# Kernel tuning notes

Measured on AMD Instinct MI355X. Metric: run time of the kernel, lower is better.

## Reference

```python
import jax, jax.numpy as jnp
import numpy as np

B, T, C, D = 8, 4096, 1024, 64  # batch, block_size, input_dim, output_dim


def setup_inputs() -> dict:
    key = jax.random.key(0)
    kx, kk, kq, kv = jax.random.split(key, 4)
    s = 1.0 / np.sqrt(C)  # nn.Linear default init range scale
    X = jax.random.normal(kx, (B, T, C), dtype=jnp.float32)
    Wk = jax.random.uniform(kk, (D, C), jnp.float32, -s, s) * 0.01  # key weight scaled by 0.01 per __post_init__
    Wq = jax.random.uniform(kq, (D, C), jnp.float32, -s, s)
    Wv = jax.random.uniform(kv, (D, C), jnp.float32, -s, s)
    return {"X": X, "Wk": Wk, "Wq": Wq, "Wv": Wv}


def reference(X, Wk, Wq, Wv):
    # bias-free linear projections (torch Linear: X @ W.T)
    keys = jnp.einsum('btc,dc->btd', X, Wk)
    queries = jnp.einsum('btc,dc->btd', X, Wq)
    values = jnp.einsum('btc,dc->btd', X, Wv)
    # scaled dot-product logits [B, T, T]
    logits = jnp.einsum('btd,bsd->bts', queries, keys) / jnp.sqrt(jnp.float32(D))
    causal = jnp.tril(jnp.ones((T, T), dtype=bool))
    logits = jnp.where(causal[None, :, :], logits, -jnp.inf)
    affinities = jax.nn.softmax(logits, axis=2)  # dropout_frac=0.0 -> identity
    return jnp.einsum('bts,bsd->btd', affinities, values)
```

## Files before the change

kernel.cpp:

```cpp
#include <hip/hip_runtime.h>


typedef short bf16x8 __attribute__((ext_vector_type(8)));
typedef short bf16x4 __attribute__((ext_vector_type(4)));
typedef float f32x4  __attribute__((ext_vector_type(4)));

static __device__ __forceinline__ short f2bf(float x) {
    union { float f; unsigned u; } v; v.f = x;
    return (short)((v.u + 0x7fffu + ((v.u >> 16) & 1u)) >> 16);
}

__global__ __launch_bounds__(256, 2) void proj_kernel(
    const float* __restrict__ X,
    const float* __restrict__ Wk, const float* __restrict__ Wq,
    const float* __restrict__ Wv,
    short* __restrict__ Kb,
    short* __restrict__ Qb,
    short* __restrict__ Vt)
{
    __shared__ __align__(16) short xs[2][64 * 72];
    const int tid  = threadIdx.x;
    const int w    = tid >> 6;
    const int lane = tid & 63;
    const int l15  = lane & 15;
    const int quad = lane >> 4;
    const int t0   = blockIdx.x * 64;

    const int rowA = tid >> 3, colg = tid & 7;
    const int rowB = rowA + 32;
    const float* xpA = X + (long)(t0 + rowA) * 1024 + colg * 8;
    const float* xpB = X + (long)(t0 + rowB) * 1024 + colg * 8;
    const int lwA = rowA * 72 + colg * 8;
    const int lwB = rowB * 72 + colg * 8;

    const float* wbase[3];
    wbase[0] = Wk + (long)(w * 16 + l15) * 1024 + quad * 8;
    wbase[1] = Wq + (long)(w * 16 + l15) * 1024 + quad * 8;
    wbase[2] = Wv + (long)(w * 16 + l15) * 1024 + quad * 8;

    f32x4 acc[4][3];
#pragma unroll
    for (int rt = 0; rt < 4; ++rt)
#pragma unroll
        for (int m = 0; m < 3; ++m) { acc[rt][m][0]=0.f; acc[rt][m][1]=0.f; acc[rt][m][2]=0.f; acc[rt][m][3]=0.f; }

    f32x4 xr[2][4];
    bf16x8 wfc[3][2], wfn[3][2];

    {
#pragma unroll
        for (int s = 0; s < 2; ++s) {
            const int k0 = s * 64;
            xr[s][0] = *(const f32x4*)(xpA + k0);
            xr[s][1] = *(const f32x4*)(xpA + k0 + 4);
            xr[s][2] = *(const f32x4*)(xpB + k0);
            xr[s][3] = *(const f32x4*)(xpB + k0 + 4);
        }
#pragma unroll
        for (int m = 0; m < 3; ++m) {
            const float sc = (m == 1) ? 0.18033688f : 1.0f;
#pragma unroll
            for (int k2 = 0; k2 < 2; ++k2) {
                f32x4 w0 = *(const f32x4*)(wbase[m] + k2 * 32);
                f32x4 w1 = *(const f32x4*)(wbase[m] + k2 * 32 + 4);
                bf16x8 f;
#pragma unroll
                for (int j = 0; j < 4; ++j) { f[j] = f2bf(w0[j] * sc); f[j + 4] = f2bf(w1[j] * sc); }
                wfc[m][k2] = f;
            }
        }
        bf16x8 c0, c1;
#pragma unroll
        for (int j = 0; j < 4; ++j) { c0[j] = f2bf(xr[0][0][j]); c0[j+4] = f2bf(xr[0][1][j]);
                                      c1[j] = f2bf(xr[0][2][j]); c1[j+4] = f2bf(xr[0][3][j]); }
        *(bf16x8*)(&xs[0][lwA]) = c0;
        *(bf16x8*)(&xs[0][lwB]) = c1;
    }
    __syncthreads();

#pragma unroll 2
    for (int ks = 0; ks < 16; ++ks) {
        const int buf = ks & 1;
        if (ks < 14) {
            const int k0 = (ks + 2) * 64;
            xr[buf][0] = *(const f32x4*)(xpA + k0);
            xr[buf][1] = *(const f32x4*)(xpA + k0 + 4);
            xr[buf][2] = *(const f32x4*)(xpB + k0);
            xr[buf][3] = *(const f32x4*)(xpB + k0 + 4);
        }
        f32x4 wr[3][2][2];
        if (ks < 15) {
            const int k0 = (ks + 1) * 64;
#pragma unroll
            for (int m = 0; m < 3; ++m)
#pragma unroll
                for (int k2 = 0; k2 < 2; ++k2) {
                    wr[m][k2][0] = *(const f32x4*)(wbase[m] + k0 + k2 * 32);
                    wr[m][k2][1] = *(const f32x4*)(wbase[m] + k0 + k2 * 32 + 4);
                }
        }
#pragma unroll
        for (int k2 = 0; k2 < 2; ++k2)
#pragma unroll
            for (int rt = 0; rt < 4; ++rt) {
                bf16x8 a = *(const bf16x8*)(&xs[buf][(rt * 16 + l15) * 72 + k2 * 32 + quad * 8]);
#pragma unroll
                for (int m = 0; m < 3; ++m)
                    acc[rt][m] = __builtin_amdgcn_mfma_f32_16x16x32_bf16(a, wfc[m][k2], acc[rt][m], 0, 0, 0);
            }
        if (ks < 15) {
#pragma unroll
            for (int m = 0; m < 3; ++m) {
                const float sc = (m == 1) ? 0.18033688f : 1.0f;
#pragma unroll
                for (int k2 = 0; k2 < 2; ++k2) {
                    bf16x8 f;
#pragma unroll
                    for (int j = 0; j < 4; ++j) { f[j] = f2bf(wr[m][k2][0][j] * sc); f[j + 4] = f2bf(wr[m][k2][1][j] * sc); }
                    wfn[m][k2] = f;
                }
            }
            const int nset = (ks + 1) & 1;
            bf16x8 c0, c1;
#pragma unroll
            for (int j = 0; j < 4; ++j) { c0[j] = f2bf(xr[nset][0][j]); c0[j+4] = f2bf(xr[nset][1][j]);
                                          c1[j] = f2bf(xr[nset][2][j]); c1[j+4] = f2bf(xr[nset][3][j]); }
            *(bf16x8*)(&xs[nset][lwA]) = c0;
            *(bf16x8*)(&xs[nset][lwB]) = c1;
        }
        __syncthreads();
#pragma unroll
        for (int m = 0; m < 3; ++m)
#pragma unroll
            for (int k2 = 0; k2 < 2; ++k2) wfc[m][k2] = wfn[m][k2];
    }

    const int d    = w * 16 + l15;
    const int bidx = t0 >> 12;
#pragma unroll
    for (int rt = 0; rt < 4; ++rt) {
        const int tf = t0 + rt * 16 + quad * 4;
#pragma unroll
        for (int r = 0; r < 4; ++r) Kb[(long)(tf + r) * 64 + d] = f2bf(acc[rt][0][r]);
#pragma unroll
        for (int r = 0; r < 4; ++r) Qb[(long)(tf + r) * 64 + d] = f2bf(acc[rt][1][r]);
        bf16x4 pv;
#pragma unroll
        for (int r = 0; r < 4; ++r) pv[r] = f2bf(acc[rt][2][r]);
        *(bf16x4*)(Vt + ((long)bidx * 64 + d) * 4096 + (tf & 4095)) = pv;
    }
}

__global__ __launch_bounds__(256, 2) void flash_kernel(
    const short* __restrict__ Qb,
    const short* __restrict__ Kb,
    const short* __restrict__ Vt,
    float* __restrict__ Out)
{
    __shared__ __align__(16) char smem[33280];
    short* ps = (short*)smem;
    float* os = (float*)smem;
    float* ls = (float*)(smem + 32768);

    const int tid  = threadIdx.x;
    const int w    = tid >> 6;
    const int lane = tid & 63;
    const int l15  = lane & 15;
    const int quad = lane >> 4;
    const int b    = blockIdx.x & 7;
    const int tile = 127 - (blockIdx.x >> 3);
    const int t0   = tile * 32;

    const int nkb = (t0 >> 6) + 1;
    const int len = (nkb + 3) >> 2;
    const int kb0 = w * len;
    const int kb1 = (kb0 + len < nkb) ? (kb0 + len) : nkb;

    const short* Kbase = Kb + (long)b * 4096 * 64;
    const short* Vbase = Vt + (long)b * 64 * 4096;

    bf16x8 aq[2][2];
#pragma unroll
    for (int q2 = 0; q2 < 2; ++q2) {
        const long qoff = ((long)b * 4096 + t0 + q2 * 16 + l15) * 64;
        aq[q2][0] = *(const bf16x8*)(Qb + qoff + quad * 8);
        aq[q2][1] = *(const bf16x8*)(Qb + qoff + 32 + quad * 8);
    }

    bf16x8 bones;
#pragma unroll
    for (int j = 0; j < 8; ++j) bones[j] = (l15 == 0) ? (short)0x3F80 : (short)0;

    f32x4 o[2][4], lacc[2];
#pragma unroll
    for (int q2 = 0; q2 < 2; ++q2) {
        lacc[q2][0]=0.f; lacc[q2][1]=0.f; lacc[q2][2]=0.f; lacc[q2][3]=0.f;
#pragma unroll
        for (int dt = 0; dt < 4; ++dt) { o[q2][dt][0]=0.f; o[q2][dt][1]=0.f; o[q2][dt][2]=0.f; o[q2][dt][3]=0.f; }
    }

    bf16x8 kc[4][2], kn[4][2];
    if (kb0 < kb1) {
        const int s0 = kb0 << 6;
#pragma unroll
        for (int ct = 0; ct < 4; ++ct) {
            const short* kp = Kbase + (long)(s0 + ct * 16 + l15) * 64 + quad * 8;
            kc[ct][0] = *(const bf16x8*)(kp);
            kc[ct][1] = *(const bf16x8*)(kp + 32);
        }
    }

    for (int kb = kb0; kb < kb1; ++kb) {
        const int s0 = kb << 6;

        bf16x8 vf[4][2];
#pragma unroll
        for (int dt = 0; dt < 4; ++dt) {
            const short* vp = Vbase + (long)(dt * 16 + l15) * 4096 + s0 + quad * 8;
            vf[dt][0] = *(const bf16x8*)(vp);
            vf[dt][1] = *(const bf16x8*)(vp + 32);
        }
        if (kb + 1 < kb1) {
            const int sn = s0 + 64;
#pragma unroll
            for (int ct = 0; ct < 4; ++ct) {
                const short* kp = Kbase + (long)(sn + ct * 16 + l15) * 64 + quad * 8;
                kn[ct][0] = *(const bf16x8*)(kp);
                kn[ct][1] = *(const bf16x8*)(kp + 32);
            }
        }

#pragma unroll
        for (int q2 = 0; q2 < 2; ++q2) {
            short* myps = ps + ((w << 1) | q2) * 1152;
            f32x4 st[4];
#pragma unroll
            for (int ct = 0; ct < 4; ++ct) {
                f32x4 z; z[0]=0.f; z[1]=0.f; z[2]=0.f; z[3]=0.f;
                z = __builtin_amdgcn_mfma_f32_16x16x32_bf16(aq[q2][0], kc[ct][0], z, 0, 0, 0);
                st[ct] = __builtin_amdgcn_mfma_f32_16x16x32_bf16(aq[q2][1], kc[ct][1], st[ct] = z, 0, 0, 0);
            }
            if (kb == nkb - 1) {
#pragma unroll
                for (int ct = 0; ct < 4; ++ct) {
                    const int s = s0 + ct * 16 + l15;
#pragma unroll
                    for (int r = 0; r < 4; ++r)
                        if (s > t0 + q2 * 16 + quad * 4 + r) st[ct][r] = -1e30f;
                }
            }
#pragma unroll
            for (int ct = 0; ct < 4; ++ct)
#pragma unroll
                for (int r = 0; r < 4; ++r)
                    myps[(quad * 4 + r) * 72 + ct * 16 + l15] =
                        f2bf(__builtin_amdgcn_exp2f(st[ct][r]));
            bf16x8 ap0 = *(const bf16x8*)(myps + l15 * 72 + quad * 8);
            bf16x8 ap1 = *(const bf16x8*)(myps + l15 * 72 + 32 + quad * 8);
            lacc[q2] = __builtin_amdgcn_mfma_f32_16x16x32_bf16(ap0, bones, lacc[q2], 0, 0, 0);
            lacc[q2] = __builtin_amdgcn_mfma_f32_16x16x32_bf16(ap1, bones, lacc[q2], 0, 0, 0);
#pragma unroll
            for (int dt = 0; dt < 4; ++dt) {
                o[q2][dt] = __builtin_amdgcn_mfma_f32_16x16x32_bf16(ap0, vf[dt][0], o[q2][dt], 0, 0, 0);
                o[q2][dt] = __builtin_amdgcn_mfma_f32_16x16x32_bf16(ap1, vf[dt][1], o[q2][dt], 0, 0, 0);
            }
        }
#pragma unroll
        for (int ct = 0; ct < 4; ++ct) { kc[ct][0] = kn[ct][0]; kc[ct][1] = kn[ct][1]; }
    }

    __syncthreads();
#pragma unroll
    for (int q2 = 0; q2 < 2; ++q2) {
#pragma unroll
        for (int dt = 0; dt < 4; ++dt)
#pragma unroll
            for (int r = 0; r < 4; ++r)
                os[w * 2048 + (q2 * 16 + quad * 4 + r) * 64 + dt * 16 + l15] = o[q2][dt][r];
        if (l15 == 0) {
#pragma unroll
            for (int r = 0; r < 4; ++r) ls[w * 32 + q2 * 16 + quad * 4 + r] = lacc[q2][r];
        }
    }
    __syncthreads();

    const int row = tid >> 3, c0 = (tid & 7) * 8;
    f32x4 a0, a1; a0[0]=0.f;a0[1]=0.f;a0[2]=0.f;a0[3]=0.f; a1=a0;
    float lsum = 0.f;
#pragma unroll
    for (int w2 = 0; w2 < 4; ++w2) {
        f32x4 v0 = *(const f32x4*)(os + w2 * 2048 + row * 64 + c0);
        f32x4 v1 = *(const f32x4*)(os + w2 * 2048 + row * 64 + c0 + 4);
        a0[0]+=v0[0]; a0[1]+=v0[1]; a0[2]+=v0[2]; a0[3]+=v0[3];
        a1[0]+=v1[0]; a1[1]+=v1[1]; a1[2]+=v1[2]; a1[3]+=v1[3];
        lsum += ls[w2 * 32 + row];
    }
    const float inv = 1.0f / lsum;
    f32x4 r0, r1;
    r0[0]=a0[0]*inv; r0[1]=a0[1]*inv; r0[2]=a0[2]*inv; r0[3]=a0[3]*inv;
    r1[0]=a1[0]*inv; r1[1]=a1[1]*inv; r1[2]=a1[2]*inv; r1[3]=a1[3]*inv;
    float* op = Out + ((long)b * 4096 + t0 + row) * 64 + c0;
    *(f32x4*)(op)     = r0;
    *(f32x4*)(op + 4) = r1;
}

extern "C" void kernel_launch(void* const* d_in, const int* in_sizes, int n_in,
                              void* d_out, int out_size, void* d_ws, size_t ws_size,
                              hipStream_t stream) {
    const float* X  = (const float*)d_in[0];
    const float* Wk = (const float*)d_in[1];
    const float* Wq = (const float*)d_in[2];
    const float* Wv = (const float*)d_in[3];

    short* ws = (short*)d_ws;
    const long NE = (long)8 * 4096 * 64;
    short* Qb = ws;
    short* Kb = ws + NE;
    short* Vt = ws + 2 * NE;

    proj_kernel<<<512, 256, 0, stream>>>(X, Wk, Wq, Wv, Kb, Qb, Vt);
    flash_kernel<<<1024, 256, 0, stream>>>(Qb, Kb, Vt, (float*)d_out);
}
```

Measured before the change: 291.5 us.

## Pre-convert weights to bf16 and restructure projection to per-wave register tiles

A new small kernel converts Wk/Wq/Wv to bf16 once, folding the query scale in, and the projection kernel reads these bf16 weights directly. The projection kernel no longer stages X through shared memory; each wave now owns 32 rows and computes all 192 output columns, with a 4-deep register prefetch of X. This removes repeated weight conversion and the block-wide barriers, at the cost of more accumulator registers, more redundant global weight traffic and an extra launch. The flash kernel's loop is also reordered to batch both query subtiles' score MFMAs and softmax writes, and launch-bound occupancy hints are dropped.

```diff
diff --git a/kernel.cpp b/kernel.cpp
--- a/kernel.cpp
+++ b/kernel.cpp
@@ -10,148 +10,104 @@
     return (short)((v.u + 0x7fffu + ((v.u >> 16) & 1u)) >> 16);
 }
 
-__global__ __launch_bounds__(256, 2) void proj_kernel(
+__global__ __launch_bounds__(256) void wconv_kernel(
+    const float* __restrict__ Wk, const float* __restrict__ Wq,
+    const float* __restrict__ Wv, short* __restrict__ Wc)
+{
+    const int i = (blockIdx.x * 256 + threadIdx.x) * 4;
+    const int m = i >> 16;
+    const int off = i & 65535;
+    const float* src = (m == 0) ? Wk : (m == 1) ? Wq : Wv;
+    const float s = (m == 1) ? 0.18033688f : 1.0f;
+    f32x4 v = *(const f32x4*)(src + off);
+    bf16x4 o;
+#pragma unroll
+    for (int r = 0; r < 4; ++r) o[r] = f2bf(v[r] * s);
+    *(bf16x4*)(Wc + i) = o;
+}
+
+__global__ __launch_bounds__(256) void proj_kernel(
     const float* __restrict__ X,
-    const float* __restrict__ Wk, const float* __restrict__ Wq,
-    const float* __restrict__ Wv,
+    const short* __restrict__ Wc,
     short* __restrict__ Kb,
     short* __restrict__ Qb,
     short* __restrict__ Vt)
 {
-    __shared__ __align__(16) short xs[2][64 * 72];
     const int tid  = threadIdx.x;
     const int w    = tid >> 6;
     const int lane = tid & 63;
     const int l15  = lane & 15;
     const int quad = lane >> 4;
-    const int t0   = blockIdx.x * 64;
-
-    const int rowA = tid >> 3, colg = tid & 7;
-    const int rowB = rowA + 32;
-    const float* xpA = X + (long)(t0 + rowA) * 1024 + colg * 8;
-    const float* xpB = X + (long)(t0 + rowB) * 1024 + colg * 8;
-    const int lwA = rowA * 72 + colg * 8;
-    const int lwB = rowB * 72 + colg * 8;
-
-    const float* wbase[3];
-    wbase[0] = Wk + (long)(w * 16 + l15) * 1024 + quad * 8;
-    wbase[1] = Wq + (long)(w * 16 + l15) * 1024 + quad * 8;
-    wbase[2] = Wv + (long)(w * 16 + l15) * 1024 + quad * 8;
-
-    f32x4 acc[4][3];
-#pragma unroll
-    for (int rt = 0; rt < 4; ++rt)
-#pragma unroll
-        for (int m = 0; m < 3; ++m) { acc[rt][m][0]=0.f; acc[rt][m][1]=0.f; acc[rt][m][2]=0.f; acc[rt][m][3]=0.f; }
-
-    f32x4 xr[2][4];
-    bf16x8 wfc[3][2], wfn[3][2];
-
-    {
-#pragma unroll
-        for (int s = 0; s < 2; ++s) {
-            const int k0 = s * 64;
-            xr[s][0] = *(const f32x4*)(xpA + k0);
-            xr[s][1] = *(const f32x4*)(xpA + k0 + 4);
-            xr[s][2] = *(const f32x4*)(xpB + k0);
-            xr[s][3] = *(const f32x4*)(xpB + k0 + 4);
-        }
-#pragma unroll
-        for (int m = 0; m < 3; ++m) {
-            const float sc = (m == 1) ? 0.18033688f : 1.0f;
-#pragma unroll
-            for (int k2 = 0; k2 < 2; ++k2) {
-                f32x4 w0 = *(const f32x4*)(wbase[m] + k2 * 32);
-                f32x4 w1 = *(const f32x4*)(wbase[m] + k2 * 32 + 4);
-                bf16x8 f;
-#pragma unroll
-                for (int j = 0; j < 4; ++j) { f[j] = f2bf(w0[j] * sc); f[j + 4] = f2bf(w1[j] * sc); }
-                wfc[m][k2] = f;
-            }
-        }
-        bf16x8 c0, c1;
-#pragma unroll
-        for (int j = 0; j < 4; ++j) { c0[j] = f2bf(xr[0][0][j]); c0[j+4] = f2bf(xr[0][1][j]);
-                                      c1[j] = f2bf(xr[0][2][j]); c1[j+4] = f2bf(xr[0][3][j]); }
-        *(bf16x8*)(&xs[0][lwA]) = c0;
-        *(bf16x8*)(&xs[0][lwB]) = c1;
-    }
-    __syncthreads();
-
-#pragma unroll 2
-    for (int ks = 0; ks < 16; ++ks) {
-        const int buf = ks & 1;
-        if (ks < 14) {
-            const int k0 = (ks + 2) * 64;
-            xr[buf][0] = *(const f32x4*)(xpA + k0);
-            xr[buf][1] = *(const f32x4*)(xpA + k0 + 4);
-            xr[buf][2] = *(const f32x4*)(xpB + k0);
-            xr[buf][3] = *(const f32x4*)(xpB + k0 + 4);
-        }
-        f32x4 wr[3][2][2];
-        if (ks < 15) {
-            const int k0 = (ks + 1) * 64;
-#pragma unroll
-            for (int m = 0; m < 3; ++m)
-#pragma unroll
-                for (int k2 = 0; k2 < 2; ++k2) {
-                    wr[m][k2][0] = *(const f32x4*)(wbase[m] + k0 + k2 * 32);
-                    wr[m][k2][1] = *(const f32x4*)(wbase[m] + k0 + k2 * 32 + 4);
-                }
-        }
-#pragma unroll
-        for (int k2 = 0; k2 < 2; ++k2)
-#pragma unroll
-            for (int rt = 0; rt < 4; ++rt) {
-                bf16x8 a = *(const bf16x8*)(&xs[buf][(rt * 16 + l15) * 72 + k2 * 32 + quad * 8]);
-#pragma unroll
-                for (int m = 0; m < 3; ++m)
-                    acc[rt][m] = __builtin_amdgcn_mfma_f32_16x16x32_bf16(a, wfc[m][k2], acc[rt][m], 0, 0, 0);
-            }
-        if (ks < 15) {
-#pragma unroll
-            for (int m = 0; m < 3; ++m) {
-                const float sc = (m == 1) ? 0.18033688f : 1.0f;
-#pragma unroll
-                for (int k2 = 0; k2 < 2; ++k2) {
-                    bf16x8 f;
-#pragma unroll
-                    for (int j = 0; j < 4; ++j) { f[j] = f2bf(wr[m][k2][0][j] * sc); f[j + 4] = f2bf(wr[m][k2][1][j] * sc); }
-                    wfn[m][k2] = f;
-                }
-            }
-            const int nset = (ks + 1) & 1;
-            bf16x8 c0, c1;
-#pragma unroll
-            for (int j = 0; j < 4; ++j) { c0[j] = f2bf(xr[nset][0][j]); c0[j+4] = f2bf(xr[nset][1][j]);
-                                          c1[j] = f2bf(xr[nset][2][j]); c1[j+4] = f2bf(xr[nset][3][j]); }
-            *(bf16x8*)(&xs[nset][lwA]) = c0;
-            *(bf16x8*)(&xs[nset][lwB]) = c1;
-        }
-        __syncthreads();
+    const int t0   = blockIdx.x * 128 + w * 32;
+
+    const float* xA = X + (long)(t0 + l15) * 1024 + quad * 8;
+    const float* xB = xA + 16 * 1024;
+    const short* wb = Wc + (long)l15 * 1024 + quad * 8;
+
+    f32x4 acc[2][12];
+#pragma unroll
+    for (int rt = 0; rt < 2; ++rt)
+#pragma unroll
+        for (int t = 0; t < 12; ++t) { acc[rt][t][0]=0.f; acc[rt][t][1]=0.f; acc[rt][t][2]=0.f; acc[rt][t][3]=0.f; }
+
+    f32x4 ar[4][4];
+#pragma unroll
+    for (int d = 0; d < 3; ++d) {
+        ar[d][0] = *(const f32x4*)(xA + d * 32);
+        ar[d][1] = *(const f32x4*)(xA + d * 32 + 4);
+        ar[d][2] = *(const f32x4*)(xB + d * 32);
+        ar[d][3] = *(const f32x4*)(xB + d * 32 + 4);
+    }
+
+#pragma unroll 4
+    for (int ks = 0; ks < 32; ++ks) {
+        const int cur = ks & 3;
+        if (ks + 3 < 32) {
+            const int nxt = (ks + 3) & 3;
+            ar[nxt][0] = *(const f32x4*)(xA + (ks + 3) * 32);
+            ar[nxt][1] = *(const f32x4*)(xA + (ks + 3) * 32 + 4);
+            ar[nxt][2] = *(const f32x4*)(xB + (ks + 3) * 32);
+            ar[nxt][3] = *(const f32x4*)(xB + (ks + 3) * 32 + 4);
+        }
+        bf16x8 bw[12];
 #pragma unroll
         for (int m = 0; m < 3; ++m)
 #pragma unroll
-            for (int k2 = 0; k2 < 2; ++k2) wfc[m][k2] = wfn[m][k2];
-    }
-
-    const int d    = w * 16 + l15;
+            for (int dt = 0; dt < 4; ++dt)
+                bw[m * 4 + dt] = *(const bf16x8*)(wb + m * 65536 + dt * 16384 + ks * 32);
+        bf16x8 a0, a1;
+#pragma unroll
+        for (int j = 0; j < 4; ++j) {
+            a0[j] = f2bf(ar[cur][0][j]); a0[j + 4] = f2bf(ar[cur][1][j]);
+            a1[j] = f2bf(ar[cur][2][j]); a1[j + 4] = f2bf(ar[cur][3][j]);
+        }
+#pragma unroll
+        for (int t = 0; t < 12; ++t) {
+            acc[0][t] = __builtin_amdgcn_mfma_f32_16x16x32_bf16(a0, bw[t], acc[0][t], 0, 0, 0);
+            acc[1][t] = __builtin_amdgcn_mfma_f32_16x16x32_bf16(a1, bw[t], acc[1][t], 0, 0, 0);
+        }
+    }
+
     const int bidx = t0 >> 12;
 #pragma unroll
-    for (int rt = 0; rt < 4; ++rt) {
+    for (int rt = 0; rt < 2; ++rt) {
         const int tf = t0 + rt * 16 + quad * 4;
 #pragma unroll
-        for (int r = 0; r < 4; ++r) Kb[(long)(tf + r) * 64 + d] = f2bf(acc[rt][0][r]);
-#pragma unroll
-        for (int r = 0; r < 4; ++r) Qb[(long)(tf + r) * 64 + d] = f2bf(acc[rt][1][r]);
-        bf16x4 pv;
-#pragma unroll
-        for (int r = 0; r < 4; ++r) pv[r] = f2bf(acc[rt][2][r]);
-        *(bf16x4*)(Vt + ((long)bidx * 64 + d) * 4096 + (tf & 4095)) = pv;
-    }
-}
-
-__global__ __launch_bounds__(256, 2) void flash_kernel(
+        for (int dt = 0; dt < 4; ++dt) {
+            const int d = dt * 16 + l15;
+#pragma unroll
+            for (int r = 0; r < 4; ++r) Kb[(long)(tf + r) * 64 + d] = f2bf(acc[rt][0 + dt][r]);
+#pragma unroll
+            for (int r = 0; r < 4; ++r) Qb[(long)(tf + r) * 64 + d] = f2bf(acc[rt][4 + dt][r]);
+            bf16x4 pv;
+#pragma unroll
+            for (int r = 0; r < 4; ++r) pv[r] = f2bf(acc[rt][8 + dt][r]);
+            *(bf16x4*)(Vt + ((long)bidx * 64 + d) * 4096 + (tf & 4095)) = pv;
+        }
+    }
+}
+
+__global__ __launch_bounds__(256) void flash_kernel(
     const short* __restrict__ Qb,
     const short* __restrict__ Kb,
     const short* __restrict__ Vt,
@@ -230,39 +186,55 @@
             }
         }
 
-#pragma unroll
-        for (int q2 = 0; q2 < 2; ++q2) {
-            short* myps = ps + ((w << 1) | q2) * 1152;
-            f32x4 st[4];
+        f32x4 st[2][4];
+#pragma unroll
+        for (int q2 = 0; q2 < 2; ++q2)
 #pragma unroll
             for (int ct = 0; ct < 4; ++ct) {
                 f32x4 z; z[0]=0.f; z[1]=0.f; z[2]=0.f; z[3]=0.f;
                 z = __builtin_amdgcn_mfma_f32_16x16x32_bf16(aq[q2][0], kc[ct][0], z, 0, 0, 0);
-                st[ct] = __builtin_amdgcn_mfma_f32_16x16x32_bf16(aq[q2][1], kc[ct][1], st[ct] = z, 0, 0, 0);
+                st[q2][ct] = __builtin_amdgcn_mfma_f32_16x16x32_bf16(aq[q2][1], kc[ct][1], z, 0, 0, 0);
             }
-            if (kb == nkb - 1) {
+
+        if (kb == nkb - 1) {
+#pragma unroll
+            for (int q2 = 0; q2 < 2; ++q2)
 #pragma unroll
                 for (int ct = 0; ct < 4; ++ct) {
                     const int s = s0 + ct * 16 + l15;
 #pragma unroll
                     for (int r = 0; r < 4; ++r)
-                        if (s > t0 + q2 * 16 + quad * 4 + r) st[ct][r] = -1e30f;
+                        if (s > t0 + q2 * 16 + quad * 4 + r) st[q2][ct][r] = -1e30f;
                 }
-            }
+        }
+
+#pragma unroll
+        for (int q2 = 0; q2 < 2; ++q2) {
+            short* myps = ps + ((w << 1) | q2) * 1152;
 #pragma unroll
             for (int ct = 0; ct < 4; ++ct)
 #pragma unroll
                 for (int r = 0; r < 4; ++r)
                     myps[(quad * 4 + r) * 72 + ct * 16 + l15] =
-                        f2bf(__builtin_amdgcn_exp2f(st[ct][r]));
-            bf16x8 ap0 = *(const bf16x8*)(myps + l15 * 72 + quad * 8);
-            bf16x8 ap1 = *(const bf16x8*)(myps + l15 * 72 + 32 + quad * 8);
-            lacc[q2] = __builtin_amdgcn_mfma_f32_16x16x32_bf16(ap0, bones, lacc[q2], 0, 0, 0);
-            lacc[q2] = __builtin_amdgcn_mfma_f32_16x16x32_bf16(ap1, bones, lacc[q2], 0, 0, 0);
+                        f2bf(__builtin_amdgcn_exp2f(st[q2][ct][r]));
+        }
+
+        bf16x8 ap[2][2];
+#pragma unroll
+        for (int q2 = 0; q2 < 2; ++q2) {
+            short* myps = ps + ((w << 1) | q2) * 1152;
+            ap[q2][0] = *(const bf16x8*)(myps + l15 * 72 + quad * 8);
+            ap[q2][1] = *(const bf16x8*)(myps + l15 * 72 + 32 + quad * 8);
+        }
+
+#pragma unroll
+        for (int q2 = 0; q2 < 2; ++q2) {
+            lacc[q2] = __builtin_amdgcn_mfma_f32_16x16x32_bf16(ap[q2][0], bones, lacc[q2], 0, 0, 0);
+            lacc[q2] = __builtin_amdgcn_mfma_f32_16x16x32_bf16(ap[q2][1], bones, lacc[q2], 0, 0, 0);
 #pragma unroll
             for (int dt = 0; dt < 4; ++dt) {
-                o[q2][dt] = __builtin_amdgcn_mfma_f32_16x16x32_bf16(ap0, vf[dt][0], o[q2][dt], 0, 0, 0);
-                o[q2][dt] = __builtin_amdgcn_mfma_f32_16x16x32_bf16(ap1, vf[dt][1], o[q2][dt], 0, 0, 0);
+                o[q2][dt] = __builtin_amdgcn_mfma_f32_16x16x32_bf16(ap[q2][0], vf[dt][0], o[q2][dt], 0, 0, 0);
+                o[q2][dt] = __builtin_amdgcn_mfma_f32_16x16x32_bf16(ap[q2][1], vf[dt][1], o[q2][dt], 0, 0, 0);
             }
         }
 #pragma unroll
@@ -314,10 +286,12 @@
 
     short* ws = (short*)d_ws;
     const long NE = (long)8 * 4096 * 64;
-    short* Qb = ws;
-    short* Kb = ws + NE;
-    short* Vt = ws + 2 * NE;
-
-    proj_kernel<<<512, 256, 0, stream>>>(X, Wk, Wq, Wv, Kb, Qb, Vt);
+    short* Wc = ws;
+    short* Qb = ws + 196608;
+    short* Kb = Qb + NE;
+    short* Vt = Kb + NE;
+
+    wconv_kernel<<<192, 256, 0, stream>>>(Wk, Wq, Wv, Wc);
+    proj_kernel<<<256, 256, 0, stream>>>(X, Wc, Kb, Qb, Vt);
     flash_kernel<<<1024, 256, 0, stream>>>(Qb, Kb, Vt, (float*)d_out);
 }
```

Measured after the change: 305.4 us. 4.8% more time.
